# Performance work log

Measured on AMD Instinct MI355X. Metric: run time of the kernel, lower is better.

## Reference

```python
import jax, jax.numpy as jnp
import numpy as np

N, C, T, V, K = 1024, 32, 8, 64, 3
CT = C * T  # = in_channels = out_channels of the 1x1 convs


def setup_inputs() -> dict:
    key = jax.random.key(0)
    k1, k2, k3, k4 = jax.random.split(key, 4)
    x = jax.random.normal(k1, (N, C, T, V), dtype=jnp.float32)
    # stacked per-branch 1x1-conv weights (Conv2d(CT, CT, 1) == Linear over CT)
    W = jax.random.normal(k2, (K, CT, CT), dtype=jnp.float32) * (1.0 / np.sqrt(CT))
    b = jax.random.normal(k3, (K, CT), dtype=jnp.float32) * 0.01
    # learnable adjacency stack A: (K, V, V)
    A = jax.random.normal(k4, (K, V, V), dtype=jnp.float32) * 0.1
    return {"x": x, "W": W, "b": b, "A": A}


def reference(x, W, b, A):
    n, c, t, v = x.shape
    ct = c * t
    # (N,C,T,V) -> (N,V,C*T): each node's feature vector over channels*time
    xf = x.transpose(0, 3, 1, 2).reshape(n, v, ct)
    # per-branch 1x1 conv == per-branch linear over CT: (K,N,V,CT)
    y = jnp.einsum('nvc,kdc->knvd', xf, W) + b[:, None, None, :]
    # adjacency aggregation per branch, summed over branches (replaces cat+sum)
    out = jnp.einsum('knvd,kvw->nwd', y, A)  # (N,V,CT)
    # (N,V,C,T) -> (N,C,V,T), matching y.sum(-1).permute(0,1,3,2)
    return out.reshape(n, v, c, t).transpose(0, 2, 1, 3)
```

## Files before the change

kernel.cpp:

```cpp
#include <hip/hip_runtime.h>
#include <hip/hip_bf16.h>


typedef __attribute__((ext_vector_type(8))) short bf16x8;
typedef __attribute__((ext_vector_type(4))) float f32x4;

#define RAWBAR() asm volatile("s_waitcnt lgkmcnt(0)\n\ts_barrier" ::: "memory")

__device__ __forceinline__ short f2bf(float f) {
  union { float f; unsigned u; } c; c.f = f;
  unsigned r = c.u + 0x7FFFu + ((c.u >> 16) & 1u);
  return (short)(r >> 16);
}

__device__ __forceinline__ unsigned pkbf(float a, float b) {
  float2 t; t.x = a; t.y = b;
  union { __hip_bfloat162 h; unsigned u; } c;
  c.h = __float22bfloat162_rn(t);
  return c.u;
}

#define ASW_OFF  393216
#define BIAS_OFF 417792

__global__ __launch_bounds__(256) void prep_kernel(
    const float* __restrict__ W, const float* __restrict__ b,
    const float* __restrict__ A, short* __restrict__ Wsw,
    short* __restrict__ Asw, float* __restrict__ biasCM) {
  int t = blockIdx.x * 256 + threadIdx.x;
  if (t < 196608) {
    int e = t & 7, l = (t >> 3) & 63, ks = (t >> 9) & 7, mt = (t >> 12) & 3,
        wv = (t >> 14) & 3, k = t >> 16;
    int d = 64 * wv + 16 * mt + (l & 15);
    int c = 32 * ks + 8 * (l >> 4) + e;
    Wsw[t] = f2bf(W[(k * 256 + d) * 256 + c]);
  } else if (t < 196608 + 12288) {
    int t2 = t - 196608;
    int e = t2 & 7, l = (t2 >> 3) & 63, nt = (t2 >> 9) & 3, ks = (t2 >> 11) & 1,
        k = t2 >> 12;
    int w = nt * 16 + (l & 15);
    int v = ks * 32 + (l >> 4) * 8 + e;
    Asw[t2] = f2bf(A[(k * 64 + v) * 64 + w]);
  } else {
    int t2 = t - 196608 - 12288;
    int w = t2 >> 8, d = t2 & 255;
    float s = 0.f;
    for (int k = 0; k < 3; ++k) {
      float cs = 0.f;
#pragma unroll
      for (int v = 0; v < 64; ++v) cs += A[(k * 64 + v) * 64 + w];
      s += cs * b[k * 256 + d];
    }
    biasCM[t2] = s;
  }
}

#define UT_STRIDE 264

__device__ __forceinline__ void stage1(
    const short* __restrict__ Asw, int k, const bf16x8 (&xf)[2][4],
    short* __restrict__ Utw, int wv, int lane, int li, int lq) {
  const short* AswK = Asw + k * 4096;
  f32x4 acc1[4][4];
#pragma unroll
  for (int mt = 0; mt < 4; ++mt)
#pragma unroll
    for (int nt = 0; nt < 4; ++nt)
      acc1[mt][nt] = (f32x4){0.f, 0.f, 0.f, 0.f};

#pragma unroll
  for (int ks = 0; ks < 2; ++ks) {
    bf16x8 bfr[4];
#pragma unroll
    for (int nt = 0; nt < 4; ++nt)
      bfr[nt] = *(const bf16x8*)(AswK + ((ks * 4 + nt) * 64 + lane) * 8);
#pragma unroll
    for (int mt = 0; mt < 4; ++mt)
#pragma unroll
      for (int nt = 0; nt < 4; ++nt)
        acc1[mt][nt] = __builtin_amdgcn_mfma_f32_16x16x32_bf16(
            xf[ks][mt], bfr[nt], acc1[mt][nt], 0, 0, 0);
  }

#pragma unroll
  for (int mt = 0; mt < 4; ++mt)
#pragma unroll
    for (int nt = 0; nt < 4; ++nt) {
      int w = nt * 16 + li;
      int ct = 64 * wv + 16 * mt + 4 * lq;
      union { unsigned u[2]; unsigned long long ull; } p;
      p.u[0] = pkbf(acc1[mt][nt][0], acc1[mt][nt][1]);
      p.u[1] = pkbf(acc1[mt][nt][2], acc1[mt][nt][3]);
      *(unsigned long long*)(&Utw[w * UT_STRIDE + ct]) = p.ull;
    }
}

__global__ __launch_bounds__(256, 2) void gcn_main(
    const float* __restrict__ x, const short* __restrict__ Wsw,
    const short* __restrict__ Asw, const float* __restrict__ biasCM,
    float* __restrict__ out) {
  __shared__ short Ut[64 * UT_STRIDE];

  const int tid = threadIdx.x;
  const int wv = tid >> 6;
  const int lane = tid & 63;
  const int li = lane & 15;
  const int lq = lane >> 4;
  const int n = blockIdx.x;

  const float* xn = x + (size_t)n * 16384;
  float* outn = out + (size_t)n * 16384;

  f32x4 acc2[4][4];
#pragma unroll
  for (int mt = 0; mt < 4; ++mt)
#pragma unroll
    for (int nt = 0; nt < 4; ++nt) {
      const float4 bb = *(const float4*)(biasCM + (nt * 16 + li) * 256 +
                                         64 * wv + 16 * mt + 4 * lq);
      acc2[mt][nt] = (f32x4){bb.x, bb.y, bb.z, bb.w};
    }

  bf16x8 xf[2][4];
#pragma unroll
  for (int ks = 0; ks < 2; ++ks)
#pragma unroll
    for (int mt = 0; mt < 4; ++mt) {
      const float4* p =
          (const float4*)(xn + (64 * wv + 16 * mt + li) * 64 + 32 * ks + 8 * lq);
      float4 f0 = p[0], f1 = p[1];
      union { bf16x8 v; unsigned u[4]; } t;
      t.u[0] = pkbf(f0.x, f0.y); t.u[1] = pkbf(f0.z, f0.w);
      t.u[2] = pkbf(f1.x, f1.y); t.u[3] = pkbf(f1.z, f1.w);
      xf[ks][mt] = t.v;
    }

  stage1(Asw, 0, xf, Ut, wv, lane, li, lq);

  bf16x8 awA[4], awB[4];
  {
    const short* W0 = Wsw + (0 * 4 + wv) * 16384;
#pragma unroll
    for (int mt = 0; mt < 4; ++mt) {
      awA[mt] = *(const bf16x8*)(W0 + ((mt * 8 + 0) * 64 + lane) * 8);
      awB[mt] = *(const bf16x8*)(W0 + ((mt * 8 + 1) * 64 + lane) * 8);
    }
  }

  RAWBAR();

#pragma unroll
  for (int k = 0; k < 3; ++k) {
    const short* WswK = Wsw + (k * 4 + wv) * 16384;
    const short* WswN = Wsw + ((k + 1) * 4 + wv) * 16384;

#pragma unroll
    for (int ks = 0; ks < 8; ++ks) {
      bf16x8 bu[4];
#pragma unroll
      for (int nt = 0; nt < 4; ++nt)
        bu[nt] = *(const bf16x8*)(&Ut[(nt * 16 + li) * UT_STRIDE + 32 * ks + 8 * lq]);

      bf16x8 aw0[4];
#pragma unroll
      for (int mt = 0; mt < 4; ++mt) aw0[mt] = (ks & 1) ? awB[mt] : awA[mt];

      if (ks < 6) {
#pragma unroll
        for (int mt = 0; mt < 4; ++mt) {
          bf16x8 nv = *(const bf16x8*)(WswK + ((mt * 8 + ks + 2) * 64 + lane) * 8);
          if (ks & 1) awB[mt] = nv; else awA[mt] = nv;
        }
      } else if (k < 2) {
#pragma unroll
        for (int mt = 0; mt < 4; ++mt) {
          bf16x8 nv = *(const bf16x8*)(WswN + ((mt * 8 + (ks - 6)) * 64 + lane) * 8);
          if (ks & 1) awB[mt] = nv; else awA[mt] = nv;
        }
      }

#pragma unroll
      for (int mt = 0; mt < 4; ++mt)
#pragma unroll
        for (int nt = 0; nt < 4; ++nt)
          acc2[mt][nt] = __builtin_amdgcn_mfma_f32_16x16x32_bf16(
              aw0[mt], bu[nt], acc2[mt][nt], 0, 0, 0);
    }

    if (k < 2) {
      RAWBAR();
      stage1(Asw, k + 1, xf, Ut, wv, lane, li, lq);
      RAWBAR();
    }
  }

#pragma unroll
  for (int mt = 0; mt < 4; ++mt)
#pragma unroll
    for (int nt = 0; nt < 4; ++nt) {
      float4 vv;
      vv.x = acc2[mt][nt][0];
      vv.y = acc2[mt][nt][1];
      vv.z = acc2[mt][nt][2];
      vv.w = acc2[mt][nt][3];
      *(float4*)(outn + (8 * wv + 2 * mt + (lq >> 1)) * 512 +
                 (nt * 16 + li) * 8 + 4 * (lq & 1)) = vv;
    }
}

extern "C" void kernel_launch(void* const* d_in, const int* in_sizes, int n_in,
                              void* d_out, int out_size, void* d_ws, size_t ws_size,
                              hipStream_t stream) {
  (void)in_sizes; (void)n_in; (void)out_size; (void)ws_size;
  const float* x = (const float*)d_in[0];
  const float* W = (const float*)d_in[1];
  const float* b = (const float*)d_in[2];
  const float* A = (const float*)d_in[3];
  float* out = (float*)d_out;

  short* Wsw = (short*)d_ws;
  short* Asw = (short*)((char*)d_ws + ASW_OFF);
  float* biasCM = (float*)((char*)d_ws + BIAS_OFF);

  prep_kernel<<<880, 256, 0, stream>>>(W, b, A, Wsw, Asw, biasCM);
  gcn_main<<<1024, 256, 0, stream>>>(x, Wsw, Asw, biasCM, out);
}
```

Before: 147.7 us.

## Process two samples per block with rotated branch order and persistent W prefetch

Halves the grid so each block handles two batch samples in turn. The block's branch order is rotated by block index so different blocks read different W slices at the same moment. The W register prefetch carries across the sample boundary, and the second sample's x is loaded before the last stage2 of the first. This amortizes block launch and setup and spreads L2 traffic, but 512 blocks may underfill the GPU compared with 1024 and lengthen the serial chain per block.

```diff
diff --git a/kernel.cpp b/kernel.cpp
--- a/kernel.cpp
+++ b/kernel.cpp
@@ -95,33 +95,47 @@
     }
 }
 
-__global__ __launch_bounds__(256, 2) void gcn_main(
-    const float* __restrict__ x, const short* __restrict__ Wsw,
-    const short* __restrict__ Asw, const float* __restrict__ biasCM,
-    float* __restrict__ out) {
-  __shared__ short Ut[64 * UT_STRIDE];
-
-  const int tid = threadIdx.x;
-  const int wv = tid >> 6;
-  const int lane = tid & 63;
-  const int li = lane & 15;
-  const int lq = lane >> 4;
-  const int n = blockIdx.x;
-
-  const float* xn = x + (size_t)n * 16384;
-  float* outn = out + (size_t)n * 16384;
-
-  f32x4 acc2[4][4];
-#pragma unroll
-  for (int mt = 0; mt < 4; ++mt)
-#pragma unroll
-    for (int nt = 0; nt < 4; ++nt) {
-      const float4 bb = *(const float4*)(biasCM + (nt * 16 + li) * 256 +
-                                         64 * wv + 16 * mt + 4 * lq);
-      acc2[mt][nt] = (f32x4){bb.x, bb.y, bb.z, bb.w};
-    }
-
-  bf16x8 xf[2][4];
+__device__ __forceinline__ void stage2_8(
+    const short* __restrict__ Ut, const short* __restrict__ WswK,
+    const short* __restrict__ WswR, bf16x8 (&awA)[4], bf16x8 (&awB)[4],
+    f32x4 (&acc2)[4][4], int li, int lq, int lane) {
+#pragma unroll
+  for (int ks = 0; ks < 8; ++ks) {
+    bf16x8 bu[4];
+#pragma unroll
+    for (int nt = 0; nt < 4; ++nt)
+      bu[nt] = *(const bf16x8*)(&Ut[(nt * 16 + li) * UT_STRIDE + 32 * ks + 8 * lq]);
+
+    bf16x8 aw0[4];
+#pragma unroll
+    for (int mt = 0; mt < 4; ++mt) aw0[mt] = (ks & 1) ? awB[mt] : awA[mt];
+
+    if (ks < 6) {
+#pragma unroll
+      for (int mt = 0; mt < 4; ++mt) {
+        bf16x8 nv = *(const bf16x8*)(WswK + ((mt * 8 + ks + 2) * 64 + lane) * 8);
+        if (ks & 1) awB[mt] = nv; else awA[mt] = nv;
+      }
+    } else if (WswR) {
+#pragma unroll
+      for (int mt = 0; mt < 4; ++mt) {
+        bf16x8 nv = *(const bf16x8*)(WswR + ((mt * 8 + (ks - 6)) * 64 + lane) * 8);
+        if (ks & 1) awB[mt] = nv; else awA[mt] = nv;
+      }
+    }
+
+#pragma unroll
+    for (int mt = 0; mt < 4; ++mt)
+#pragma unroll
+      for (int nt = 0; nt < 4; ++nt)
+        acc2[mt][nt] = __builtin_amdgcn_mfma_f32_16x16x32_bf16(
+            aw0[mt], bu[nt], acc2[mt][nt], 0, 0, 0);
+  }
+}
+
+__device__ __forceinline__ void load_xf(const float* __restrict__ xn,
+                                        bf16x8 (&xf)[2][4], int wv, int li,
+                                        int lq) {
 #pragma unroll
   for (int ks = 0; ks < 2; ++ks)
 #pragma unroll
@@ -134,66 +148,24 @@
       t.u[2] = pkbf(f1.x, f1.y); t.u[3] = pkbf(f1.z, f1.w);
       xf[ks][mt] = t.v;
     }
-
-  stage1(Asw, 0, xf, Ut, wv, lane, li, lq);
-
-  bf16x8 awA[4], awB[4];
-  {
-    const short* W0 = Wsw + (0 * 4 + wv) * 16384;
-#pragma unroll
-    for (int mt = 0; mt < 4; ++mt) {
-      awA[mt] = *(const bf16x8*)(W0 + ((mt * 8 + 0) * 64 + lane) * 8);
-      awB[mt] = *(const bf16x8*)(W0 + ((mt * 8 + 1) * 64 + lane) * 8);
-    }
-  }
-
-  RAWBAR();
-
-#pragma unroll
-  for (int k = 0; k < 3; ++k) {
-    const short* WswK = Wsw + (k * 4 + wv) * 16384;
-    const short* WswN = Wsw + ((k + 1) * 4 + wv) * 16384;
-
-#pragma unroll
-    for (int ks = 0; ks < 8; ++ks) {
-      bf16x8 bu[4];
-#pragma unroll
-      for (int nt = 0; nt < 4; ++nt)
-        bu[nt] = *(const bf16x8*)(&Ut[(nt * 16 + li) * UT_STRIDE + 32 * ks + 8 * lq]);
-
-      bf16x8 aw0[4];
-#pragma unroll
-      for (int mt = 0; mt < 4; ++mt) aw0[mt] = (ks & 1) ? awB[mt] : awA[mt];
-
-      if (ks < 6) {
-#pragma unroll
-        for (int mt = 0; mt < 4; ++mt) {
-          bf16x8 nv = *(const bf16x8*)(WswK + ((mt * 8 + ks + 2) * 64 + lane) * 8);
-          if (ks & 1) awB[mt] = nv; else awA[mt] = nv;
-        }
-      } else if (k < 2) {
-#pragma unroll
-        for (int mt = 0; mt < 4; ++mt) {
-          bf16x8 nv = *(const bf16x8*)(WswN + ((mt * 8 + (ks - 6)) * 64 + lane) * 8);
-          if (ks & 1) awB[mt] = nv; else awA[mt] = nv;
-        }
-      }
-
-#pragma unroll
-      for (int mt = 0; mt < 4; ++mt)
-#pragma unroll
-        for (int nt = 0; nt < 4; ++nt)
-          acc2[mt][nt] = __builtin_amdgcn_mfma_f32_16x16x32_bf16(
-              aw0[mt], bu[nt], acc2[mt][nt], 0, 0, 0);
-    }
-
-    if (k < 2) {
-      RAWBAR();
-      stage1(Asw, k + 1, xf, Ut, wv, lane, li, lq);
-      RAWBAR();
-    }
-  }
-
+}
+
+__device__ __forceinline__ void load_bias(const float* __restrict__ biasCM,
+                                          f32x4 (&acc2)[4][4], int wv, int li,
+                                          int lq) {
+#pragma unroll
+  for (int mt = 0; mt < 4; ++mt)
+#pragma unroll
+    for (int nt = 0; nt < 4; ++nt) {
+      const float4 bb = *(const float4*)(biasCM + (nt * 16 + li) * 256 +
+                                         64 * wv + 16 * mt + 4 * lq);
+      acc2[mt][nt] = (f32x4){bb.x, bb.y, bb.z, bb.w};
+    }
+}
+
+__device__ __forceinline__ void store_out(float* __restrict__ outn,
+                                          const f32x4 (&acc2)[4][4], int wv,
+                                          int li, int lq) {
 #pragma unroll
   for (int mt = 0; mt < 4; ++mt)
 #pragma unroll
@@ -206,6 +178,70 @@
       *(float4*)(outn + (8 * wv + 2 * mt + (lq >> 1)) * 512 +
                  (nt * 16 + li) * 8 + 4 * (lq & 1)) = vv;
     }
+}
+
+__global__ __launch_bounds__(256, 2) void gcn_main(
+    const float* __restrict__ x, const short* __restrict__ Wsw,
+    const short* __restrict__ Asw, const float* __restrict__ biasCM,
+    float* __restrict__ out) {
+  __shared__ short Ut[64 * UT_STRIDE];
+
+  const int tid = threadIdx.x;
+  const int wv = tid >> 6;
+  const int lane = tid & 63;
+  const int li = lane & 15;
+  const int lq = lane >> 4;
+
+  const int bid = blockIdx.x;
+  const int k0 = bid % 3;
+  const int k1 = (k0 + 1 < 3) ? k0 + 1 : 0;
+  const int k2 = (k1 + 1 < 3) ? k1 + 1 : 0;
+
+  const short* Wk0 = Wsw + (k0 * 4 + wv) * 16384;
+  const short* Wk1 = Wsw + (k1 * 4 + wv) * 16384;
+  const short* Wk2 = Wsw + (k2 * 4 + wv) * 16384;
+
+  const float* xn1 = x + (size_t)bid * 16384;
+  const float* xn2 = x + (size_t)(bid + 512) * 16384;
+  float* out1 = out + (size_t)bid * 16384;
+  float* out2 = out + (size_t)(bid + 512) * 16384;
+
+  bf16x8 xf[2][4];
+  load_xf(xn1, xf, wv, li, lq);
+  f32x4 acc2[4][4];
+  load_bias(biasCM, acc2, wv, li, lq);
+  stage1(Asw, k0, xf, Ut, wv, lane, li, lq);
+
+  bf16x8 awA[4], awB[4];
+#pragma unroll
+  for (int mt = 0; mt < 4; ++mt) {
+    awA[mt] = *(const bf16x8*)(Wk0 + ((mt * 8 + 0) * 64 + lane) * 8);
+    awB[mt] = *(const bf16x8*)(Wk0 + ((mt * 8 + 1) * 64 + lane) * 8);
+  }
+  RAWBAR();
+
+  stage2_8(Ut, Wk0, Wk1, awA, awB, acc2, li, lq, lane);
+  RAWBAR();  stage1(Asw, k1, xf, Ut, wv, lane, li, lq);  RAWBAR();
+  stage2_8(Ut, Wk1, Wk2, awA, awB, acc2, li, lq, lane);
+  RAWBAR();  stage1(Asw, k2, xf, Ut, wv, lane, li, lq);  RAWBAR();
+
+  bf16x8 xf2[2][4];
+  load_xf(xn2, xf2, wv, li, lq);
+
+  stage2_8(Ut, Wk2, Wk0, awA, awB, acc2, li, lq, lane);
+  store_out(out1, acc2, wv, li, lq);
+
+  load_bias(biasCM, acc2, wv, li, lq);
+  RAWBAR();
+  stage1(Asw, k0, xf2, Ut, wv, lane, li, lq);
+  RAWBAR();
+
+  stage2_8(Ut, Wk0, Wk1, awA, awB, acc2, li, lq, lane);
+  RAWBAR();  stage1(Asw, k1, xf2, Ut, wv, lane, li, lq);  RAWBAR();
+  stage2_8(Ut, Wk1, Wk2, awA, awB, acc2, li, lq, lane);
+  RAWBAR();  stage1(Asw, k2, xf2, Ut, wv, lane, li, lq);  RAWBAR();
+  stage2_8(Ut, Wk2, nullptr, awA, awB, acc2, li, lq, lane);
+  store_out(out2, acc2, wv, li, lq);
 }
 
 extern "C" void kernel_launch(void* const* d_in, const int* in_sizes, int n_in,
@@ -223,5 +259,5 @@
   float* biasCM = (float*)((char*)d_ws + BIAS_OFF);
 
   prep_kernel<<<880, 256, 0, stream>>>(W, b, A, Wsw, Asw, biasCM);
-  gcn_main<<<1024, 256, 0, stream>>>(x, Wsw, Asw, biasCM, out);
-}
+  gcn_main<<<512, 256, 0, stream>>>(x, Wsw, Asw, biasCM, out);
+}
```

Result: slower. 160.5 us (+8.7%).

## Cut register pressure to raise occupancy: reload x per stage, drop W prefetch

Applied to the files above, without the earlier changes.

Stops keeping the bf16 x fragments live across the whole kernel. They are reloaded from global memory and converted inside each stage1 call, one mt tile at a time, so stage1 only needs a 4-tile accumulator. The double-buffered W register prefetch is removed and W fragments are loaded just in time. Launch bounds change from 2 to 4 waves per SIMD so more blocks can run concurrently. The cost is that x is re-read and re-converted three times, and W load latency is no longer hidden by the software pipeline but has to be covered by the extra occupancy.

```diff
diff --git a/kernel.cpp b/kernel.cpp
--- a/kernel.cpp
+++ b/kernel.cpp
@@ -58,44 +58,49 @@
 #define UT_STRIDE 264
 
 __device__ __forceinline__ void stage1(
-    const short* __restrict__ Asw, int k, const bf16x8 (&xf)[2][4],
+    const float* __restrict__ xn, const short* __restrict__ Asw, int k,
     short* __restrict__ Utw, int wv, int lane, int li, int lq) {
   const short* AswK = Asw + k * 4096;
-  f32x4 acc1[4][4];
 #pragma unroll
-  for (int mt = 0; mt < 4; ++mt)
+  for (int mt = 0; mt < 4; ++mt) {
+    bf16x8 xk[2];
 #pragma unroll
-    for (int nt = 0; nt < 4; ++nt)
-      acc1[mt][nt] = (f32x4){0.f, 0.f, 0.f, 0.f};
+    for (int ks = 0; ks < 2; ++ks) {
+      const float4* p =
+          (const float4*)(xn + (64 * wv + 16 * mt + li) * 64 + 32 * ks + 8 * lq);
+      float4 f0 = p[0], f1 = p[1];
+      union { bf16x8 v; unsigned u[4]; } t;
+      t.u[0] = pkbf(f0.x, f0.y); t.u[1] = pkbf(f0.z, f0.w);
+      t.u[2] = pkbf(f1.x, f1.y); t.u[3] = pkbf(f1.z, f1.w);
+      xk[ks] = t.v;
+    }
+
+    f32x4 acc1[4];
+#pragma unroll
+    for (int nt = 0; nt < 4; ++nt) acc1[nt] = (f32x4){0.f, 0.f, 0.f, 0.f};
 
 #pragma unroll
-  for (int ks = 0; ks < 2; ++ks) {
-    bf16x8 bfr[4];
+    for (int ks = 0; ks < 2; ++ks)
 #pragma unroll
-    for (int nt = 0; nt < 4; ++nt)
-      bfr[nt] = *(const bf16x8*)(AswK + ((ks * 4 + nt) * 64 + lane) * 8);
-#pragma unroll
-    for (int mt = 0; mt < 4; ++mt)
-#pragma unroll
-      for (int nt = 0; nt < 4; ++nt)
-        acc1[mt][nt] = __builtin_amdgcn_mfma_f32_16x16x32_bf16(
-            xf[ks][mt], bfr[nt], acc1[mt][nt], 0, 0, 0);
-  }
+      for (int nt = 0; nt < 4; ++nt) {
+        bf16x8 bfr = *(const bf16x8*)(AswK + ((ks * 4 + nt) * 64 + lane) * 8);
+        acc1[nt] = __builtin_amdgcn_mfma_f32_16x16x32_bf16(
+            xk[ks], bfr, acc1[nt], 0, 0, 0);
+      }
 
-#pragma unroll
-  for (int mt = 0; mt < 4; ++mt)
 #pragma unroll
     for (int nt = 0; nt < 4; ++nt) {
       int w = nt * 16 + li;
       int ct = 64 * wv + 16 * mt + 4 * lq;
       union { unsigned u[2]; unsigned long long ull; } p;
-      p.u[0] = pkbf(acc1[mt][nt][0], acc1[mt][nt][1]);
-      p.u[1] = pkbf(acc1[mt][nt][2], acc1[mt][nt][3]);
+      p.u[0] = pkbf(acc1[nt][0], acc1[nt][1]);
+      p.u[1] = pkbf(acc1[nt][2], acc1[nt][3]);
       *(unsigned long long*)(&Utw[w * UT_STRIDE + ct]) = p.ull;
     }
+  }
 }
 
-__global__ __launch_bounds__(256, 2) void gcn_main(
+__global__ __launch_bounds__(256, 4) void gcn_main(
     const float* __restrict__ x, const short* __restrict__ Wsw,
     const short* __restrict__ Asw, const float* __restrict__ biasCM,
     float* __restrict__ out) {
@@ -121,75 +126,34 @@
       acc2[mt][nt] = (f32x4){bb.x, bb.y, bb.z, bb.w};
     }
 
-  bf16x8 xf[2][4];
-#pragma unroll
-  for (int ks = 0; ks < 2; ++ks)
-#pragma unroll
-    for (int mt = 0; mt < 4; ++mt) {
-      const float4* p =
-          (const float4*)(xn + (64 * wv + 16 * mt + li) * 64 + 32 * ks + 8 * lq);
-      float4 f0 = p[0], f1 = p[1];
-      union { bf16x8 v; unsigned u[4]; } t;
-      t.u[0] = pkbf(f0.x, f0.y); t.u[1] = pkbf(f0.z, f0.w);
-      t.u[2] = pkbf(f1.x, f1.y); t.u[3] = pkbf(f1.z, f1.w);
-      xf[ks][mt] = t.v;
-    }
-
-  stage1(Asw, 0, xf, Ut, wv, lane, li, lq);
-
-  bf16x8 awA[4], awB[4];
-  {
-    const short* W0 = Wsw + (0 * 4 + wv) * 16384;
-#pragma unroll
-    for (int mt = 0; mt < 4; ++mt) {
-      awA[mt] = *(const bf16x8*)(W0 + ((mt * 8 + 0) * 64 + lane) * 8);
-      awB[mt] = *(const bf16x8*)(W0 + ((mt * 8 + 1) * 64 + lane) * 8);
-    }
-  }
-
+  stage1(xn, Asw, 0, Ut, wv, lane, li, lq);
   RAWBAR();
 
 #pragma unroll
   for (int k = 0; k < 3; ++k) {
     const short* WswK = Wsw + (k * 4 + wv) * 16384;
-    const short* WswN = Wsw + ((k + 1) * 4 + wv) * 16384;
 
 #pragma unroll
     for (int ks = 0; ks < 8; ++ks) {
-      bf16x8 bu[4];
+      bf16x8 aw[4], bu[4];
+#pragma unroll
+      for (int mt = 0; mt < 4; ++mt)
+        aw[mt] = *(const bf16x8*)(WswK + ((mt * 8 + ks) * 64 + lane) * 8);
 #pragma unroll
       for (int nt = 0; nt < 4; ++nt)
         bu[nt] = *(const bf16x8*)(&Ut[(nt * 16 + li) * UT_STRIDE + 32 * ks + 8 * lq]);
-
-      bf16x8 aw0[4];
-#pragma unroll
-      for (int mt = 0; mt < 4; ++mt) aw0[mt] = (ks & 1) ? awB[mt] : awA[mt];
-
-      if (ks < 6) {
-#pragma unroll
-        for (int mt = 0; mt < 4; ++mt) {
-          bf16x8 nv = *(const bf16x8*)(WswK + ((mt * 8 + ks + 2) * 64 + lane) * 8);
-          if (ks & 1) awB[mt] = nv; else awA[mt] = nv;
-        }
-      } else if (k < 2) {
-#pragma unroll
-        for (int mt = 0; mt < 4; ++mt) {
-          bf16x8 nv = *(const bf16x8*)(WswN + ((mt * 8 + (ks - 6)) * 64 + lane) * 8);
-          if (ks & 1) awB[mt] = nv; else awA[mt] = nv;
-        }
-      }
 
 #pragma unroll
       for (int mt = 0; mt < 4; ++mt)
 #pragma unroll
         for (int nt = 0; nt < 4; ++nt)
           acc2[mt][nt] = __builtin_amdgcn_mfma_f32_16x16x32_bf16(
-              aw0[mt], bu[nt], acc2[mt][nt], 0, 0, 0);
+              aw[mt], bu[nt], acc2[mt][nt], 0, 0, 0);
     }
 
     if (k < 2) {
       RAWBAR();
-      stage1(Asw, k + 1, xf, Ut, wv, lane, li, lq);
+      stage1(xn, Asw, k + 1, Ut, wv, lane, li, lq);
       RAWBAR();
     }
   }
```

Measured after the change: 211.6 us. 1.43x slower.

## Process two samples per block to reuse W fragments across samples

Applied to the files above, without the earlier changes.

Each block now handles two batch samples, each with its own LDS buffer. Every W fragment loaded from global memory feeds MFMAs for both samples, which halves weight traffic per sample. Stage1 now reloads x from global on every branch instead of keeping the bf16 x fragments in registers, and the double-buffered W prefetch is dropped. The cost is twice the accumulator registers and LDS per block, plus 512 blocks instead of 1024, which may reduce occupancy and latency hiding.

```diff
diff --git a/kernel.cpp b/kernel.cpp
--- a/kernel.cpp
+++ b/kernel.cpp
@@ -58,68 +58,9 @@
 #define UT_STRIDE 264
 
 __device__ __forceinline__ void stage1(
-    const short* __restrict__ Asw, int k, const bf16x8 (&xf)[2][4],
+    const float* __restrict__ xn, const short* __restrict__ Asw, int k,
     short* __restrict__ Utw, int wv, int lane, int li, int lq) {
   const short* AswK = Asw + k * 4096;
-  f32x4 acc1[4][4];
-#pragma unroll
-  for (int mt = 0; mt < 4; ++mt)
-#pragma unroll
-    for (int nt = 0; nt < 4; ++nt)
-      acc1[mt][nt] = (f32x4){0.f, 0.f, 0.f, 0.f};
-
-#pragma unroll
-  for (int ks = 0; ks < 2; ++ks) {
-    bf16x8 bfr[4];
-#pragma unroll
-    for (int nt = 0; nt < 4; ++nt)
-      bfr[nt] = *(const bf16x8*)(AswK + ((ks * 4 + nt) * 64 + lane) * 8);
-#pragma unroll
-    for (int mt = 0; mt < 4; ++mt)
-#pragma unroll
-      for (int nt = 0; nt < 4; ++nt)
-        acc1[mt][nt] = __builtin_amdgcn_mfma_f32_16x16x32_bf16(
-            xf[ks][mt], bfr[nt], acc1[mt][nt], 0, 0, 0);
-  }
-
-#pragma unroll
-  for (int mt = 0; mt < 4; ++mt)
-#pragma unroll
-    for (int nt = 0; nt < 4; ++nt) {
-      int w = nt * 16 + li;
-      int ct = 64 * wv + 16 * mt + 4 * lq;
-      union { unsigned u[2]; unsigned long long ull; } p;
-      p.u[0] = pkbf(acc1[mt][nt][0], acc1[mt][nt][1]);
-      p.u[1] = pkbf(acc1[mt][nt][2], acc1[mt][nt][3]);
-      *(unsigned long long*)(&Utw[w * UT_STRIDE + ct]) = p.ull;
-    }
-}
-
-__global__ __launch_bounds__(256, 2) void gcn_main(
-    const float* __restrict__ x, const short* __restrict__ Wsw,
-    const short* __restrict__ Asw, const float* __restrict__ biasCM,
-    float* __restrict__ out) {
-  __shared__ short Ut[64 * UT_STRIDE];
-
-  const int tid = threadIdx.x;
-  const int wv = tid >> 6;
-  const int lane = tid & 63;
-  const int li = lane & 15;
-  const int lq = lane >> 4;
-  const int n = blockIdx.x;
-
-  const float* xn = x + (size_t)n * 16384;
-  float* outn = out + (size_t)n * 16384;
-
-  f32x4 acc2[4][4];
-#pragma unroll
-  for (int mt = 0; mt < 4; ++mt)
-#pragma unroll
-    for (int nt = 0; nt < 4; ++nt) {
-      const float4 bb = *(const float4*)(biasCM + (nt * 16 + li) * 256 +
-                                         64 * wv + 16 * mt + 4 * lq);
-      acc2[mt][nt] = (f32x4){bb.x, bb.y, bb.z, bb.w};
-    }
 
   bf16x8 xf[2][4];
 #pragma unroll
@@ -135,65 +76,43 @@
       xf[ks][mt] = t.v;
     }
 
-  stage1(Asw, 0, xf, Ut, wv, lane, li, lq);
-
-  bf16x8 awA[4], awB[4];
-  {
-    const short* W0 = Wsw + (0 * 4 + wv) * 16384;
-#pragma unroll
-    for (int mt = 0; mt < 4; ++mt) {
-      awA[mt] = *(const bf16x8*)(W0 + ((mt * 8 + 0) * 64 + lane) * 8);
-      awB[mt] = *(const bf16x8*)(W0 + ((mt * 8 + 1) * 64 + lane) * 8);
-    }
+  f32x4 acc1[4][4];
+#pragma unroll
+  for (int mt = 0; mt < 4; ++mt)
+#pragma unroll
+    for (int nt = 0; nt < 4; ++nt)
+      acc1[mt][nt] = (f32x4){0.f, 0.f, 0.f, 0.f};
+
+#pragma unroll
+  for (int ks = 0; ks < 2; ++ks) {
+    bf16x8 bfr[4];
+#pragma unroll
+    for (int nt = 0; nt < 4; ++nt)
+      bfr[nt] = *(const bf16x8*)(AswK + ((ks * 4 + nt) * 64 + lane) * 8);
+#pragma unroll
+    for (int mt = 0; mt < 4; ++mt)
+#pragma unroll
+      for (int nt = 0; nt < 4; ++nt)
+        acc1[mt][nt] = __builtin_amdgcn_mfma_f32_16x16x32_bf16(
+            xf[ks][mt], bfr[nt], acc1[mt][nt], 0, 0, 0);
   }
 
-  RAWBAR();
-
-#pragma unroll
-  for (int k = 0; k < 3; ++k) {
-    const short* WswK = Wsw + (k * 4 + wv) * 16384;
-    const short* WswN = Wsw + ((k + 1) * 4 + wv) * 16384;
-
-#pragma unroll
-    for (int ks = 0; ks < 8; ++ks) {
-      bf16x8 bu[4];
-#pragma unroll
-      for (int nt = 0; nt < 4; ++nt)
-        bu[nt] = *(const bf16x8*)(&Ut[(nt * 16 + li) * UT_STRIDE + 32 * ks + 8 * lq]);
-
-      bf16x8 aw0[4];
-#pragma unroll
-      for (int mt = 0; mt < 4; ++mt) aw0[mt] = (ks & 1) ? awB[mt] : awA[mt];
-
-      if (ks < 6) {
-#pragma unroll
-        for (int mt = 0; mt < 4; ++mt) {
-          bf16x8 nv = *(const bf16x8*)(WswK + ((mt * 8 + ks + 2) * 64 + lane) * 8);
-          if (ks & 1) awB[mt] = nv; else awA[mt] = nv;
-        }
-      } else if (k < 2) {
-#pragma unroll
-        for (int mt = 0; mt < 4; ++mt) {
-          bf16x8 nv = *(const bf16x8*)(WswN + ((mt * 8 + (ks - 6)) * 64 + lane) * 8);
-          if (ks & 1) awB[mt] = nv; else awA[mt] = nv;
-        }
-      }
-
-#pragma unroll
-      for (int mt = 0; mt < 4; ++mt)
-#pragma unroll
-        for (int nt = 0; nt < 4; ++nt)
-          acc2[mt][nt] = __builtin_amdgcn_mfma_f32_16x16x32_bf16(
-              aw0[mt], bu[nt], acc2[mt][nt], 0, 0, 0);
-    }
-
-    if (k < 2) {
-      RAWBAR();
-      stage1(Asw, k + 1, xf, Ut, wv, lane, li, lq);
-      RAWBAR();
-    }
-  }
-
+#pragma unroll
+  for (int mt = 0; mt < 4; ++mt)
+#pragma unroll
+    for (int nt = 0; nt < 4; ++nt) {
+      int w = nt * 16 + li;
+      int ct = 64 * wv + 16 * mt + 4 * lq;
+      union { unsigned u[2]; unsigned long long ull; } p;
+      p.u[0] = pkbf(acc1[mt][nt][0], acc1[mt][nt][1]);
+      p.u[1] = pkbf(acc1[mt][nt][2], acc1[mt][nt][3]);
+      *(unsigned long long*)(&Utw[w * UT_STRIDE + ct]) = p.ull;
+    }
+}
+
+__device__ __forceinline__ void store_out(float* __restrict__ outn,
+                                          const f32x4 (&acc2)[4][4], int wv,
+                                          int li, int lq) {
 #pragma unroll
   for (int mt = 0; mt < 4; ++mt)
 #pragma unroll
@@ -206,6 +125,87 @@
       *(float4*)(outn + (8 * wv + 2 * mt + (lq >> 1)) * 512 +
                  (nt * 16 + li) * 8 + 4 * (lq & 1)) = vv;
     }
+}
+
+__global__ __launch_bounds__(256, 2) void gcn_main(
+    const float* __restrict__ x, const short* __restrict__ Wsw,
+    const short* __restrict__ Asw, const float* __restrict__ biasCM,
+    float* __restrict__ out) {
+  __shared__ short Ut1[64 * UT_STRIDE];
+  __shared__ short Ut2[64 * UT_STRIDE];
+
+  const int tid = threadIdx.x;
+  const int wv = tid >> 6;
+  const int lane = tid & 63;
+  const int li = lane & 15;
+  const int lq = lane >> 4;
+
+  const int n1 = blockIdx.x;
+  const int n2 = blockIdx.x + 512;
+
+  const float* x1 = x + (size_t)n1 * 16384;
+  const float* x2 = x + (size_t)n2 * 16384;
+
+  f32x4 acc2a[4][4], acc2b[4][4];
+#pragma unroll
+  for (int mt = 0; mt < 4; ++mt)
+#pragma unroll
+    for (int nt = 0; nt < 4; ++nt) {
+      const float4 bb = *(const float4*)(biasCM + (nt * 16 + li) * 256 +
+                                         64 * wv + 16 * mt + 4 * lq);
+      acc2a[mt][nt] = (f32x4){bb.x, bb.y, bb.z, bb.w};
+      acc2b[mt][nt] = acc2a[mt][nt];
+    }
+
+  stage1(x1, Asw, 0, Ut1, wv, lane, li, lq);
+  __builtin_amdgcn_sched_barrier(0);
+  stage1(x2, Asw, 0, Ut2, wv, lane, li, lq);
+  RAWBAR();
+
+#pragma unroll
+  for (int k = 0; k < 3; ++k) {
+    const short* WswK = Wsw + (k * 4 + wv) * 16384;
+
+#pragma unroll
+    for (int ks = 0; ks < 8; ++ks) {
+      bf16x8 aw[4];
+#pragma unroll
+      for (int mt = 0; mt < 4; ++mt)
+        aw[mt] = *(const bf16x8*)(WswK + ((mt * 8 + ks) * 64 + lane) * 8);
+
+      bf16x8 bu[4];
+#pragma unroll
+      for (int nt = 0; nt < 4; ++nt)
+        bu[nt] = *(const bf16x8*)(&Ut1[(nt * 16 + li) * UT_STRIDE + 32 * ks + 8 * lq]);
+#pragma unroll
+      for (int mt = 0; mt < 4; ++mt)
+#pragma unroll
+        for (int nt = 0; nt < 4; ++nt)
+          acc2a[mt][nt] = __builtin_amdgcn_mfma_f32_16x16x32_bf16(
+              aw[mt], bu[nt], acc2a[mt][nt], 0, 0, 0);
+
+#pragma unroll
+      for (int nt = 0; nt < 4; ++nt)
+        bu[nt] = *(const bf16x8*)(&Ut2[(nt * 16 + li) * UT_STRIDE + 32 * ks + 8 * lq]);
+#pragma unroll
+      for (int mt = 0; mt < 4; ++mt)
+#pragma unroll
+        for (int nt = 0; nt < 4; ++nt)
+          acc2b[mt][nt] = __builtin_amdgcn_mfma_f32_16x16x32_bf16(
+              aw[mt], bu[nt], acc2b[mt][nt], 0, 0, 0);
+    }
+
+    if (k < 2) {
+      RAWBAR();
+      stage1(x1, Asw, k + 1, Ut1, wv, lane, li, lq);
+      __builtin_amdgcn_sched_barrier(0);
+      stage1(x2, Asw, k + 1, Ut2, wv, lane, li, lq);
+      RAWBAR();
+    }
+  }
+
+  store_out(out + (size_t)n1 * 16384, acc2a, wv, li, lq);
+  store_out(out + (size_t)n2 * 16384, acc2b, wv, li, lq);
 }
 
 extern "C" void kernel_launch(void* const* d_in, const int* in_sizes, int n_in,
@@ -223,5 +223,5 @@
   float* biasCM = (float*)((char*)d_ws + BIAS_OFF);
 
   prep_kernel<<<880, 256, 0, stream>>>(W, b, A, Wsw, Asw, biasCM);
-  gcn_main<<<1024, 256, 0, stream>>>(x, Wsw, Asw, biasCM, out);
-}
+  gcn_main<<<512, 256, 0, stream>>>(x, Wsw, Asw, biasCM, out);
+}
```

Measured after the change: 182.7 us. +23.7%, slower.
